# Kernel tuning notes

Hardware: AMD Instinct MI355X
Metric: run time of the kernel (lower is better)

## Reference

```python
import jax, jax.numpy as jnp
import numpy as np

N_NODES = 20000   # batch of nodes (vectorized version of per-node calls)
N_SAMPLE = 32     # num_sample neighbors per node
EMBED_DIM = 256
TABLE_SIZE = 100000


def setup_inputs() -> dict:
    key = jax.random.key(0)
    k1, k2, k3, k4, k5, k6, k7, k8, k9 = jax.random.split(key, 9)
    D = EMBED_DIM
    scale = 1.0 / np.sqrt(D)
    return {
        "node_ids": jax.random.randint(k1, (N_NODES,), 0, TABLE_SIZE),
        "neigh_ids": jax.random.randint(k2, (N_NODES, N_SAMPLE), 0, TABLE_SIZE),
        "feat_table": jax.random.normal(k3, (TABLE_SIZE, D), dtype=jnp.float32),
        "Wq": jax.random.uniform(k4, (D, D), jnp.float32, -scale, scale),
        "bq": jax.random.uniform(k5, (D,), jnp.float32, -scale, scale),
        "Wk": jax.random.uniform(k6, (D, D), jnp.float32, -scale, scale),
        "bk": jax.random.uniform(k7, (D,), jnp.float32, -scale, scale),
        "Wv": jax.random.uniform(k8, (D, D), jnp.float32, -scale, scale),
        "bv": jax.random.uniform(k9, (D,), jnp.float32, -scale, scale),
    }


def reference(node_ids, neigh_ids, feat_table, Wq, bq, Wk, bk, Wv, bv):
    # id2feat lookups
    self_feats = feat_table[node_ids]            # [N, D]
    neigh_feats = feat_table[neigh_ids]          # [N, S, D]
    # context = cat(self, neighbors) along the key/value axis
    ctx = jnp.concatenate([self_feats[:, None, :], neigh_feats], axis=1)  # [N, S+1, D]
    # torch Linear: y = x @ W^T + b
    Q = self_feats @ Wq.T + bq                   # [N, D]
    K = ctx @ Wk.T + bk                          # [N, S+1, D]
    V = ctx @ Wv.T + bv                          # [N, S+1, D]
    scores = jnp.einsum('nd,nkd->nk', Q, K)      # [N, S+1]
    attn = jax.nn.softmax(scores, axis=-1)
    mix = jnp.einsum('nk,nkd->nd', attn, V)      # [N, D]
    out = jnp.tanh(mix)
    # F.normalize(p=2, dim=-1) with eps=1e-12 clamp
    norm = jnp.maximum(jnp.linalg.norm(out, axis=-1, keepdims=True), 1e-12)
    return out / norm
```

## Files before the change

kernel.cpp:

```cpp
#include <hip/hip_runtime.h>
#include <hip/hip_bf16.h>

#define D 256

typedef __bf16 bf16x8 __attribute__((ext_vector_type(8)));
typedef float  f32x4  __attribute__((ext_vector_type(4)));
typedef unsigned short ushort8v __attribute__((ext_vector_type(8)));

static __device__ __forceinline__ unsigned short f2bf_rne(float f) {
    unsigned u = __float_as_uint(f);
    u += 0x7fff + ((u >> 16) & 1);
    return (unsigned short)(u >> 16);
}
static __device__ __forceinline__ float bf2f(unsigned short h) {
    return __uint_as_float(((unsigned)h) << 16);
}
static __device__ __forceinline__ unsigned short f2h(float f) {
    _Float16 h = (_Float16)f;
    unsigned short u; __builtin_memcpy(&u, &h, 2); return u;
}
static __device__ __forceinline__ float h2f(unsigned short u) {
    _Float16 h; __builtin_memcpy(&h, &u, 2); return (float)h;
}

static __device__ __forceinline__ void cp16(const unsigned short* g, unsigned short* l) {
    __builtin_amdgcn_global_load_lds(
        (const __attribute__((address_space(1))) void*)g,
        (__attribute__((address_space(3))) void*)l, 16, 0, 0);
}

static __device__ __forceinline__ void split8(float4 a, float4 b,
                                              ushort8v& h, ushort8v& l) {
    float v[8] = {a.x, a.y, a.z, a.w, b.x, b.y, b.z, b.w};
    #pragma unroll
    for (int i = 0; i < 8; ++i) {
        unsigned short hh = f2bf_rne(v[i]);
        h[i] = hh;
        l[i] = f2bf_rne(v[i] - bf2f(hh));
    }
}

__global__ __launch_bounds__(256) void convert_all(
    const float* __restrict__ feat, int T, int nbf,
    const float* __restrict__ Wq, const float* __restrict__ Wk,
    const float* __restrict__ Wv, const float* __restrict__ bq,
    unsigned short* __restrict__ f16tab,
    unsigned short* __restrict__ wqT_h, unsigned short* __restrict__ wqT_l,
    unsigned short* __restrict__ wkT_h, unsigned short* __restrict__ wkT_l,
    unsigned short* __restrict__ wv_h,  unsigned short* __restrict__ wv_l,
    float* __restrict__ wstar)
{
    const int bx = blockIdx.x;
    if (bx < nbf) {
        const int w = threadIdx.x >> 6, l = threadIdx.x & 63;
        const int row = bx * 4 + w;
        if (row >= T) return;
        float4 v = ((const float4*)(feat + (size_t)row * D))[l];
        ushort4 h;
        h.x = f2h(v.x); h.y = f2h(v.y); h.z = f2h(v.z); h.w = f2h(v.w);
        ((ushort4*)(f16tab + (size_t)row * D))[l] = h;
        return;
    }
    const int wb = bx - nbf;
    if (wb == 256) {
        int k = threadIdx.x;
        float s = 0.f;
        for (int n = 0; n < D; ++n) s = fmaf(Wk[n * D + k], bq[n], s);
        wstar[k] = s;
        return;
    }
    int i = wb * 256 + threadIdx.x;
    int r = i >> 8, cc = i & 255;
    int ti = cc * D + r;
    float q = Wq[i]; unsigned short qh = f2bf_rne(q);
    wqT_h[ti] = qh; wqT_l[ti] = f2bf_rne(q - bf2f(qh));
    float k = Wk[i]; unsigned short kh = f2bf_rne(k);
    wkT_h[ti] = kh; wkT_l[ti] = f2bf_rne(k - bf2f(kh));
    float v = Wv[i]; unsigned short vh = f2bf_rne(v);
    wv_h[i] = vh; wv_l[i] = f2bf_rne(v - bf2f(vh));
}

template <bool BF16PAIR_OUT, bool AF32>
__global__ __launch_bounds__(256) void mfma_gemm64(
    const unsigned short* __restrict__ Ah, const unsigned short* __restrict__ Al,
    const float* __restrict__ Af,
    const int* __restrict__ idx, int M,
    const unsigned short* __restrict__ Bh, const unsigned short* __restrict__ Bl,
    const float* __restrict__ bias,
    float* __restrict__ Cf, unsigned short* __restrict__ Ch,
    unsigned short* __restrict__ Cl, int ldc)
{
    __shared__ __align__(16) unsigned short sAh[64 * 32], sAl[64 * 32];
    __shared__ __align__(16) unsigned short sBh[128 * 32], sBl[128 * 32];

    const int t = threadIdx.x;
    const int w = t >> 6, lane = t & 63;
    const int quad = lane >> 4, mcol = lane & 15;
    const int m0 = blockIdx.x * 64, n0 = blockIdx.y * 128;
    const int wc = w * 32;

    const int arow = t >> 2;
    const int kchunk = (t & 3) * 8;

    int ar = m0 + arow; if (ar > M - 1) ar = M - 1;
    if (idx) ar = idx[ar];

    const unsigned short *aph = nullptr, *apl = nullptr;
    const float *apf = nullptr;
    if constexpr (AF32) {
        apf = Af + (size_t)ar * D + kchunk;
    } else {
        aph = Ah + (size_t)ar * D + kchunk;
        apl = Al + (size_t)ar * D + kchunk;
    }
    const unsigned short* b0h = Bh + (size_t)(n0 + arow) * D + kchunk;
    const unsigned short* b1h = Bh + (size_t)(n0 + arow + 64) * D + kchunk;
    const unsigned short* b0l = Bl + (size_t)(n0 + arow) * D + kchunk;
    const unsigned short* b1l = Bl + (size_t)(n0 + arow + 64) * D + kchunk;

    f32x4 acc[4][2];
    #pragma unroll
    for (int i = 0; i < 4; ++i)
        #pragma unroll
        for (int j = 0; j < 2; ++j) acc[i][j] = (f32x4){0.f, 0.f, 0.f, 0.f};

    #pragma unroll
    for (int kb = 0; kb < D; kb += 32) {
        cp16(b0h + kb, &sBh[w * 512]);
        cp16(b1h + kb, &sBh[w * 512 + 2048]);
        cp16(b0l + kb, &sBl[w * 512]);
        cp16(b1l + kb, &sBl[w * 512 + 2048]);
        if constexpr (AF32) {
            float4 x0 = *(const float4*)(apf + kb);
            float4 x1 = *(const float4*)(apf + kb + 4);
            ushort8v h, l;
            split8(x0, x1, h, l);
            *(ushort8v*)&sAh[arow * 32 + kchunk] = h;
            *(ushort8v*)&sAl[arow * 32 + kchunk] = l;
        } else {
            cp16(aph + kb, &sAh[w * 512]);
            cp16(apl + kb, &sAl[w * 512]);
        }
        __syncthreads();

        bf16x8 fah[4], fal[4], fbh[2], fbl[2];
        #pragma unroll
        for (int i = 0; i < 4; ++i) {
            fah[i] = *(const bf16x8*)&sAh[(i * 16 + mcol) * 32 + quad * 8];
            fal[i] = *(const bf16x8*)&sAl[(i * 16 + mcol) * 32 + quad * 8];
        }
        #pragma unroll
        for (int j = 0; j < 2; ++j) {
            fbh[j] = *(const bf16x8*)&sBh[(wc + j * 16 + mcol) * 32 + quad * 8];
            fbl[j] = *(const bf16x8*)&sBl[(wc + j * 16 + mcol) * 32 + quad * 8];
        }
        #pragma unroll
        for (int i = 0; i < 4; ++i)
            #pragma unroll
            for (int j = 0; j < 2; ++j) {
                acc[i][j] = __builtin_amdgcn_mfma_f32_16x16x32_bf16(fah[i], fbh[j], acc[i][j], 0, 0, 0);
                acc[i][j] = __builtin_amdgcn_mfma_f32_16x16x32_bf16(fah[i], fbl[j], acc[i][j], 0, 0, 0);
                acc[i][j] = __builtin_amdgcn_mfma_f32_16x16x32_bf16(fal[i], fbh[j], acc[i][j], 0, 0, 0);
            }
        __syncthreads();
    }

    float bb[2];
    #pragma unroll
    for (int j = 0; j < 2; ++j) bb[j] = bias ? bias[n0 + wc + j * 16 + mcol] : 0.f;

    #pragma unroll
    for (int i = 0; i < 4; ++i) {
        #pragma unroll
        for (int r = 0; r < 4; ++r) {
            int m = m0 + i * 16 + quad * 4 + r;
            if (m < M) {
                #pragma unroll
                for (int j = 0; j < 2; ++j) {
                    float v = acc[i][j][r] + bb[j];
                    size_t off = (size_t)m * ldc + n0 + wc + j * 16 + mcol;
                    if constexpr (BF16PAIR_OUT) {
                        unsigned short hh = f2bf_rne(v);
                        Ch[off] = hh;
                        Cl[off] = f2bf_rne(v - bf2f(hh));
                    } else {
                        Cf[off] = v;
                    }
                }
            }
        }
    }
}

template <int S>
__global__ __launch_bounds__(256) void attn_wave2(
    const int* __restrict__ node_ids, const int* __restrict__ neigh_ids,
    const float* __restrict__ G, const unsigned short* __restrict__ f16tab,
    float* __restrict__ mixf, int N)
{
    constexpr int SP1 = S + 1;
    constexpr int NP  = (SP1 + 1) / 2;
    const int w = threadIdx.x >> 6, l = threadIdx.x & 63;
    const int n = blockIdx.x * 4 + w;
    if (n >= N) return;

    const int h  = l >> 5;
    const int j  = l & 31;

    int myid = 0;
    if (l < SP1) myid = (l == 0) ? node_ids[n] : neigh_ids[(size_t)n * S + (l - 1)];

    float4 g0 = ((const float4*)(G + (size_t)n * D))[j * 2];
    float4 g1 = ((const float4*)(G + (size_t)n * D))[j * 2 + 1];
    float gv[8] = {g0.x, g0.y, g0.z, g0.w, g1.x, g1.y, g1.z, g1.w};

    ushort8v rows[NP];
    #pragma unroll
    for (int p = 0; p < NP; ++p) {
        int rix = 2 * p + h; if (rix > SP1 - 1) rix = SP1 - 1;
        int idk = __shfl(myid, rix);
        rows[p] = ((const ushort8v*)(f16tab + (size_t)idk * D))[j];
    }

    float score = -1e30f;
    #pragma unroll
    for (int p = 0; p < NP; ++p) {
        ushort8v r = rows[p];
        float s = 0.f;
        #pragma unroll
        for (int i = 0; i < 8; ++i) s = fmaf(gv[i], h2f(r[i]), s);
        #pragma unroll
        for (int off = 1; off < 32; off <<= 1) s += __shfl_xor(s, off);
        if (j == p) score = s;
    }
    const int myrow = 2 * j + h;
    if (myrow >= SP1) score = -1e30f;

    float m = score;
    #pragma unroll
    for (int off = 1; off < 64; off <<= 1) m = fmaxf(m, __shfl_xor(m, off));
    float e = (myrow < SP1) ? __expf(score - m) : 0.f;
    float s = e;
    #pragma unroll
    for (int off = 1; off < 64; off <<= 1) s += __shfl_xor(s, off);
    float attn = e / s;

    float mix[8] = {0.f, 0.f, 0.f, 0.f, 0.f, 0.f, 0.f, 0.f};
    #pragma unroll
    for (int p = 0; p < NP; ++p) {
        float a = __shfl(attn, p + (l & 32));
        ushort8v r = rows[p];
        #pragma unroll
        for (int i = 0; i < 8; ++i) mix[i] = fmaf(a, h2f(r[i]), mix[i]);
    }
    #pragma unroll
    for (int i = 0; i < 8; ++i) mix[i] += __shfl_xor(mix[i], 32);

    float4 v = {mix[4 * h + 0], mix[4 * h + 1], mix[4 * h + 2], mix[4 * h + 3]};
    ((float4*)(mixf + (size_t)n * D))[j * 2 + h] = v;
}

__global__ __launch_bounds__(256) void attn_dyn(
    const int* __restrict__ node_ids, const int* __restrict__ neigh_ids,
    const float* __restrict__ G, const unsigned short* __restrict__ f16tab,
    float* __restrict__ mixf, int S)
{
    const int n = blockIdx.x, t = threadIdx.x;
    const int w = t >> 6, l = t & 63;
    __shared__ int   ids[128];
    __shared__ float sc[128];
    const int SP1 = S + 1;
    for (int k = t; k < SP1; k += 256)
        ids[k] = (k == 0) ? node_ids[n] : neigh_ids[(size_t)n * S + k - 1];
    __syncthreads();
    float4 g = ((const float4*)(G + (size_t)n * D))[l];
    for (int k = w; k < SP1; k += 4) {
        int id = ids[k];
        ushort4 h4 = ((const ushort4*)(f16tab + (size_t)id * D))[l];
        float p = g.x * h2f(h4.x) + g.y * h2f(h4.y) +
                  g.z * h2f(h4.z) + g.w * h2f(h4.w);
        #pragma unroll
        for (int off = 32; off > 0; off >>= 1) p += __shfl_down(p, off);
        if (l == 0) sc[k] = p;
    }
    __syncthreads();
    if (t < 64) {
        float v = (t < SP1) ? sc[t] : -1e30f;
        float m = v;
        #pragma unroll
        for (int off = 32; off > 0; off >>= 1) m = fmaxf(m, __shfl_down(m, off));
        m = __shfl(m, 0);
        float e = (t < SP1) ? __expf(v - m) : 0.f;
        float s = e;
        #pragma unroll
        for (int off = 32; off > 0; off >>= 1) s += __shfl_down(s, off);
        s = __shfl(s, 0);
        if (t < SP1) sc[t] = e / s;
    }
    __syncthreads();
    float mix = 0.f;
    for (int k = 0; k < SP1; ++k)
        mix = fmaf(sc[k], h2f(f16tab[(size_t)ids[k] * D + t]), mix);
    mixf[(size_t)n * D + t] = mix;
}

__global__ __launch_bounds__(256) void tanh_norm(
    const float* __restrict__ P, float* __restrict__ out, int N)
{
    const int w = threadIdx.x >> 6, l = threadIdx.x & 63;
    const int row = blockIdx.x * 4 + w;
    if (row >= N) return;
    float4 v = ((const float4*)(P + (size_t)row * D))[l];
    float4 o;
    o.x = tanhf(v.x); o.y = tanhf(v.y); o.z = tanhf(v.z); o.w = tanhf(v.w);
    float ss = o.x * o.x + o.y * o.y + o.z * o.z + o.w * o.w;
    #pragma unroll
    for (int off = 32; off > 0; off >>= 1) ss += __shfl_down(ss, off);
    ss = __shfl(ss, 0);
    float inv = 1.0f / fmaxf(sqrtf(ss), 1e-12f);
    o.x *= inv; o.y *= inv; o.z *= inv; o.w *= inv;
    ((float4*)(out + (size_t)row * D))[l] = o;
}

extern "C" void kernel_launch(void* const* d_in, const int* in_sizes, int n_in,
                              void* d_out, int out_size, void* d_ws, size_t ws_size,
                              hipStream_t stream) {
    const int*   node_ids  = (const int*)  d_in[0];
    const int*   neigh_ids = (const int*)  d_in[1];
    const float* feat      = (const float*)d_in[2];
    const float* Wq        = (const float*)d_in[3];
    const float* bq        = (const float*)d_in[4];
    const float* Wk        = (const float*)d_in[5];
    const float* Wv        = (const float*)d_in[7];
    const float* bv        = (const float*)d_in[8];
    float*       out       = (float*)d_out;

    const int N = in_sizes[0];
    const int S = in_sizes[1] / N;
    const int T = in_sizes[2] / D;

    unsigned short* f16tab = (unsigned short*)d_ws;
    float*          G      = (float*)(f16tab + (size_t)T * D);
    float*          mixf   = G + (size_t)N * D;
    float*          P      = mixf + (size_t)N * D;
    unsigned short* wqT_h  = (unsigned short*)(P + (size_t)N * D);
    unsigned short* wqT_l  = wqT_h + D * D;
    unsigned short* wkT_h  = wqT_l + D * D;
    unsigned short* wkT_l  = wkT_h + D * D;
    unsigned short* wv_h   = wkT_l + D * D;
    unsigned short* wv_l   = wv_h + D * D;
    unsigned short* MT_h   = wv_l + D * D;
    unsigned short* MT_l   = MT_h + D * D;
    float*          wstar  = (float*)(MT_l + D * D);

    const int nbf = (T + 3) / 4;

    convert_all<<<nbf + 257, 256, 0, stream>>>(
        feat, T, nbf, Wq, Wk, Wv, bq, f16tab,
        wqT_h, wqT_l, wkT_h, wkT_l, wv_h, wv_l, wstar);

    {
        dim3 grid(4, 2);
        mfma_gemm64<true, false><<<grid, 256, 0, stream>>>(
            wkT_h, wkT_l, nullptr, nullptr, D, wqT_h, wqT_l, nullptr,
            nullptr, MT_h, MT_l, D);
    }
    {
        dim3 grid((N + 63) / 64, 2);
        mfma_gemm64<false, true><<<grid, 256, 0, stream>>>(
            nullptr, nullptr, feat, node_ids, N, MT_h, MT_l, wstar,
            G, nullptr, nullptr, D);
    }
    if (S == 32)
        attn_wave2<32><<<(N + 3) / 4, 256, 0, stream>>>(
            node_ids, neigh_ids, G, f16tab, mixf, N);
    else
        attn_dyn<<<N, 256, 0, stream>>>(node_ids, neigh_ids, G, f16tab, mixf, S);

    {
        dim3 grid((N + 63) / 64, 2);
        mfma_gemm64<false, true><<<grid, 256, 0, stream>>>(
            nullptr, nullptr, mixf, nullptr, N, wv_h, wv_l, bv,
            P, nullptr, nullptr, D);
    }
    tanh_norm<<<(N + 3) / 4, 256, 0, stream>>>(P, out, N);
}
```

Measured before the change: 286.7 us.

## Fuse tanh and L2 normalize into final V GEMM epilogue with full-width tiles

The GEMM kernel is templated on its N tile width, and the final mix@Wv GEMM now uses a 256-wide tile so one block owns whole output rows. Its epilogue applies tanh, reduces the squared norm across waves through shared memory, and writes normalized output directly. This removes the separate tanh_norm kernel and the round trip of the intermediate P buffer through global memory. The cost is a larger B tile in shared memory, more accumulator registers per wave, and half as many blocks for that GEMM.

```diff
diff --git a/kernel.cpp b/kernel.cpp
--- a/kernel.cpp
+++ b/kernel.cpp
@@ -80,8 +80,8 @@
     wv_h[i] = vh; wv_l[i] = f2bf_rne(v - bf2f(vh));
 }
 
-template <bool BF16PAIR_OUT, bool AF32>
-__global__ __launch_bounds__(256) void mfma_gemm64(
+template <int BN, bool PAIR_OUT, bool AF32, bool FUSE>
+__global__ __launch_bounds__(256) void gemm_t(
     const unsigned short* __restrict__ Ah, const unsigned short* __restrict__ Al,
     const float* __restrict__ Af,
     const int* __restrict__ idx, int M,
@@ -90,14 +90,17 @@
     float* __restrict__ Cf, unsigned short* __restrict__ Ch,
     unsigned short* __restrict__ Cl, int ldc)
 {
+    constexpr int RW = BN / 4;
+    constexpr int JT = RW / 16;
+
     __shared__ __align__(16) unsigned short sAh[64 * 32], sAl[64 * 32];
-    __shared__ __align__(16) unsigned short sBh[128 * 32], sBl[128 * 32];
+    __shared__ __align__(16) unsigned short sBh[BN * 32], sBl[BN * 32];
+    __shared__ float red[FUSE ? 256 : 4];
 
     const int t = threadIdx.x;
     const int w = t >> 6, lane = t & 63;
     const int quad = lane >> 4, mcol = lane & 15;
-    const int m0 = blockIdx.x * 64, n0 = blockIdx.y * 128;
-    const int wc = w * 32;
+    const int m0 = blockIdx.x * 64, n0 = blockIdx.y * BN;
 
     const int arow = t >> 2;
     const int kchunk = (t & 3) * 8;
@@ -113,23 +116,29 @@
         aph = Ah + (size_t)ar * D + kchunk;
         apl = Al + (size_t)ar * D + kchunk;
     }
-    const unsigned short* b0h = Bh + (size_t)(n0 + arow) * D + kchunk;
-    const unsigned short* b1h = Bh + (size_t)(n0 + arow + 64) * D + kchunk;
-    const unsigned short* b0l = Bl + (size_t)(n0 + arow) * D + kchunk;
-    const unsigned short* b1l = Bl + (size_t)(n0 + arow + 64) * D + kchunk;
-
-    f32x4 acc[4][2];
+
+    const unsigned short* bh[JT];
+    const unsigned short* bl[JT];
+    #pragma unroll
+    for (int p = 0; p < JT; ++p) {
+        int row = n0 + w * RW + p * 16 + (lane >> 2);
+        bh[p] = Bh + (size_t)row * D + kchunk;
+        bl[p] = Bl + (size_t)row * D + kchunk;
+    }
+
+    f32x4 acc[4][JT];
     #pragma unroll
     for (int i = 0; i < 4; ++i)
         #pragma unroll
-        for (int j = 0; j < 2; ++j) acc[i][j] = (f32x4){0.f, 0.f, 0.f, 0.f};
+        for (int j = 0; j < JT; ++j) acc[i][j] = (f32x4){0.f, 0.f, 0.f, 0.f};
 
     #pragma unroll
     for (int kb = 0; kb < D; kb += 32) {
-        cp16(b0h + kb, &sBh[w * 512]);
-        cp16(b1h + kb, &sBh[w * 512 + 2048]);
-        cp16(b0l + kb, &sBl[w * 512]);
-        cp16(b1l + kb, &sBl[w * 512 + 2048]);
+        #pragma unroll
+        for (int p = 0; p < JT; ++p) {
+            cp16(bh[p] + kb, &sBh[(w * RW + p * 16) * 32]);
+            cp16(bl[p] + kb, &sBl[(w * RW + p * 16) * 32]);
+        }
         if constexpr (AF32) {
             float4 x0 = *(const float4*)(apf + kb);
             float4 x1 = *(const float4*)(apf + kb + 4);
@@ -143,21 +152,21 @@
         }
         __syncthreads();
 
-        bf16x8 fah[4], fal[4], fbh[2], fbl[2];
+        bf16x8 fah[4], fal[4], fbh[JT], fbl[JT];
         #pragma unroll
         for (int i = 0; i < 4; ++i) {
             fah[i] = *(const bf16x8*)&sAh[(i * 16 + mcol) * 32 + quad * 8];
             fal[i] = *(const bf16x8*)&sAl[(i * 16 + mcol) * 32 + quad * 8];
         }
         #pragma unroll
-        for (int j = 0; j < 2; ++j) {
-            fbh[j] = *(const bf16x8*)&sBh[(wc + j * 16 + mcol) * 32 + quad * 8];
-            fbl[j] = *(const bf16x8*)&sBl[(wc + j * 16 + mcol) * 32 + quad * 8];
+        for (int j = 0; j < JT; ++j) {
+            fbh[j] = *(const bf16x8*)&sBh[(w * RW + j * 16 + mcol) * 32 + quad * 8];
+            fbl[j] = *(const bf16x8*)&sBl[(w * RW + j * 16 + mcol) * 32 + quad * 8];
         }
         #pragma unroll
         for (int i = 0; i < 4; ++i)
             #pragma unroll
-            for (int j = 0; j < 2; ++j) {
+            for (int j = 0; j < JT; ++j) {
                 acc[i][j] = __builtin_amdgcn_mfma_f32_16x16x32_bf16(fah[i], fbh[j], acc[i][j], 0, 0, 0);
                 acc[i][j] = __builtin_amdgcn_mfma_f32_16x16x32_bf16(fah[i], fbl[j], acc[i][j], 0, 0, 0);
                 acc[i][j] = __builtin_amdgcn_mfma_f32_16x16x32_bf16(fal[i], fbh[j], acc[i][j], 0, 0, 0);
@@ -165,26 +174,69 @@
         __syncthreads();
     }
 
-    float bb[2];
-    #pragma unroll
-    for (int j = 0; j < 2; ++j) bb[j] = bias ? bias[n0 + wc + j * 16 + mcol] : 0.f;
-
-    #pragma unroll
-    for (int i = 0; i < 4; ++i) {
-        #pragma unroll
-        for (int r = 0; r < 4; ++r) {
-            int m = m0 + i * 16 + quad * 4 + r;
-            if (m < M) {
+    float bb[JT];
+    #pragma unroll
+    for (int j = 0; j < JT; ++j) bb[j] = bias ? bias[n0 + w * RW + j * 16 + mcol] : 0.f;
+
+    if constexpr (FUSE) {
+        float ss[4][4];
+        #pragma unroll
+        for (int i = 0; i < 4; ++i)
+            #pragma unroll
+            for (int r = 0; r < 4; ++r) {
+                float s = 0.f;
                 #pragma unroll
-                for (int j = 0; j < 2; ++j) {
-                    float v = acc[i][j][r] + bb[j];
-                    size_t off = (size_t)m * ldc + n0 + wc + j * 16 + mcol;
-                    if constexpr (BF16PAIR_OUT) {
-                        unsigned short hh = f2bf_rne(v);
-                        Ch[off] = hh;
-                        Cl[off] = f2bf_rne(v - bf2f(hh));
-                    } else {
-                        Cf[off] = v;
+                for (int j = 0; j < JT; ++j) {
+                    float v = tanhf(acc[i][j][r] + bb[j]);
+                    acc[i][j][r] = v;
+                    s = fmaf(v, v, s);
+                }
+                #pragma unroll
+                for (int off = 1; off < 16; off <<= 1) s += __shfl_xor(s, off);
+                ss[i][r] = s;
+            }
+        if (mcol == 0) {
+            #pragma unroll
+            for (int i = 0; i < 4; ++i)
+                #pragma unroll
+                for (int r = 0; r < 4; ++r)
+                    red[(i * 16 + quad * 4 + r) * 4 + w] = ss[i][r];
+        }
+        __syncthreads();
+        #pragma unroll
+        for (int i = 0; i < 4; ++i)
+            #pragma unroll
+            for (int r = 0; r < 4; ++r) {
+                int row = i * 16 + quad * 4 + r;
+                float tot = red[row * 4] + red[row * 4 + 1] +
+                            red[row * 4 + 2] + red[row * 4 + 3];
+                float inv = 1.0f / fmaxf(sqrtf(tot), 1e-12f);
+                int m = m0 + row;
+                if (m < M) {
+                    #pragma unroll
+                    for (int j = 0; j < JT; ++j)
+                        Cf[(size_t)m * ldc + n0 + w * RW + j * 16 + mcol] =
+                            acc[i][j][r] * inv;
+                }
+            }
+    } else {
+        #pragma unroll
+        for (int i = 0; i < 4; ++i) {
+            #pragma unroll
+            for (int r = 0; r < 4; ++r) {
+                int m = m0 + i * 16 + quad * 4 + r;
+                if (m < M) {
+                    #pragma unroll
+                    for (int j = 0; j < JT; ++j) {
+                        float v = acc[i][j][r] + bb[j];
+                        size_t off = (size_t)m * ldc + n0 + w * RW + j * 16 + mcol;
+                        if constexpr (PAIR_OUT) {
+                            unsigned short hh = f2bf_rne(v);
+                            Ch[off] = hh;
+                            Cl[off] = f2bf_rne(v - bf2f(hh));
+                        } else {
+                            Cf[off] = v;
+                        }
                     }
                 }
             }
@@ -304,24 +356,6 @@
     mixf[(size_t)n * D + t] = mix;
 }
 
-__global__ __launch_bounds__(256) void tanh_norm(
-    const float* __restrict__ P, float* __restrict__ out, int N)
-{
-    const int w = threadIdx.x >> 6, l = threadIdx.x & 63;
-    const int row = blockIdx.x * 4 + w;
-    if (row >= N) return;
-    float4 v = ((const float4*)(P + (size_t)row * D))[l];
-    float4 o;
-    o.x = tanhf(v.x); o.y = tanhf(v.y); o.z = tanhf(v.z); o.w = tanhf(v.w);
-    float ss = o.x * o.x + o.y * o.y + o.z * o.z + o.w * o.w;
-    #pragma unroll
-    for (int off = 32; off > 0; off >>= 1) ss += __shfl_down(ss, off);
-    ss = __shfl(ss, 0);
-    float inv = 1.0f / fmaxf(sqrtf(ss), 1e-12f);
-    o.x *= inv; o.y *= inv; o.z *= inv; o.w *= inv;
-    ((float4*)(out + (size_t)row * D))[l] = o;
-}
-
 extern "C" void kernel_launch(void* const* d_in, const int* in_sizes, int n_in,
                               void* d_out, int out_size, void* d_ws, size_t ws_size,
                               hipStream_t stream) {
@@ -342,8 +376,7 @@
     unsigned short* f16tab = (unsigned short*)d_ws;
     float*          G      = (float*)(f16tab + (size_t)T * D);
     float*          mixf   = G + (size_t)N * D;
-    float*          P      = mixf + (size_t)N * D;
-    unsigned short* wqT_h  = (unsigned short*)(P + (size_t)N * D);
+    unsigned short* wqT_h  = (unsigned short*)(mixf + (size_t)N * D);
     unsigned short* wqT_l  = wqT_h + D * D;
     unsigned short* wkT_h  = wqT_l + D * D;
     unsigned short* wkT_l  = wkT_h + D * D;
@@ -361,13 +394,13 @@
 
     {
         dim3 grid(4, 2);
-        mfma_gemm64<true, false><<<grid, 256, 0, stream>>>(
+        gemm_t<128, true, false, false><<<grid, 256, 0, stream>>>(
             wkT_h, wkT_l, nullptr, nullptr, D, wqT_h, wqT_l, nullptr,
             nullptr, MT_h, MT_l, D);
     }
     {
         dim3 grid((N + 63) / 64, 2);
-        mfma_gemm64<false, true><<<grid, 256, 0, stream>>>(
+        gemm_t<128, false, true, false><<<grid, 256, 0, stream>>>(
             nullptr, nullptr, feat, node_ids, N, MT_h, MT_l, wstar,
             G, nullptr, nullptr, D);
     }
@@ -378,10 +411,9 @@
         attn_dyn<<<N, 256, 0, stream>>>(node_ids, neigh_ids, G, f16tab, mixf, S);
 
     {
-        dim3 grid((N + 63) / 64, 2);
-        mfma_gemm64<false, true><<<grid, 256, 0, stream>>>(
+        dim3 grid((N + 63) / 64, 1);
+        gemm_t<256, false, true, true><<<grid, 256, 0, stream>>>(
             nullptr, nullptr, mixf, nullptr, N, wv_h, wv_l, bv,
-            P, nullptr, nullptr, D);
-    }
-    tanh_norm<<<(N + 3) / 4, 256, 0, stream>>>(P, out, N);
-}
+            out, nullptr, nullptr, D);
+    }
+}
```

Result: no change. 286.2 us (-0.2%).
